# Performance work log

Measured on AMD Instinct MI355X. Metric: run time of the kernel, lower is better.

The kernel has to match this reference:

```python
import jax, jax.numpy as jnp
import numpy as np

N_HEADS = 8
NEG_INF = -1e30  # finite stand-in for -inf in masked_fill (exact 0 prob after softmax)


def apply_rotary_emb(x, cos, sin):
    # x: [B, H, T, hd]; cos/sin: [T, hd] -> broadcast over B, H
    d = x.shape[-1]
    x1, x2 = x[..., : d // 2], x[..., d // 2 :]
    x_rot = jnp.concatenate((-x2, x1), axis=-1)
    return x * cos[None, None] + x_rot * sin[None, None]


def setup_inputs() -> dict:
    key = jax.random.key(0)
    ks = jax.random.split(key, 5)
    B, T, C, hd = 4, 2048, 512, 64
    x = jax.random.normal(ks[0], (B, T, C), dtype=jnp.float32)
    cos = jax.random.uniform(ks[1], (T, hd), dtype=jnp.float32)
    sin = jax.random.uniform(ks[2], (T, hd), dtype=jnp.float32)
    # xavier_uniform-ish scale for linear weights
    W_qkv = jax.random.normal(ks[3], (3 * C, C), dtype=jnp.float32) * (1.0 / np.sqrt(C))
    W_out = jax.random.normal(ks[4], (C, C), dtype=jnp.float32) * (1.0 / np.sqrt(C))
    return {"x": x, "cos": cos, "sin": sin, "W_qkv": W_qkv, "W_out": W_out}


def reference(x, cos, sin, W_qkv, W_out):
    B, T, C = x.shape
    H = N_HEADS
    hd = C // H
    # qkv projection (torch Linear: y = x @ W^T), split into q, k, v as [B, H, T, hd]
    qkv = (x @ W_qkv.T).reshape(B, T, 3, H, hd)
    qkv = jnp.transpose(qkv, (2, 0, 3, 1, 4))
    q, k, v = qkv[0], qkv[1], qkv[2]
    # RoPE on q, k
    q = apply_rotary_emb(q, cos[:T], sin[:T])
    k = apply_rotary_emb(k, cos[:T], sin[:T])
    scale = jnp.sqrt(jnp.float32(hd))
    attn = jnp.einsum("bhqd,bhkd->bhqk", q, k) / scale  # [B, H, T, T]
    causal = jnp.tril(jnp.ones((T, T), dtype=bool))
    attn = jnp.where(causal[None, None], attn, NEG_INF)
    attn = jax.nn.softmax(attn, axis=-1)
    out = jnp.einsum("bhqk,bhkd->bhqd", attn, v)  # [B, H, T, hd]
    out = jnp.transpose(out, (0, 2, 1, 3)).reshape(B, T, C)
    return out @ W_out.T
```

## Files before the change

### kernel.cpp

```cpp
#include <hip/hip_runtime.h>
#include <hip/hip_bf16.h>
#include <math.h>

#define B_SZ 4
#define T_SZ 2048
#define C_SZ 512
#define H_SZ 8
#define HD 64
#define QSCALE 0.1803368801111137f

typedef __bf16 bf16;
typedef __bf16 bf16x8 __attribute__((ext_vector_type(8)));
typedef float f32x4 __attribute__((ext_vector_type(4)));

__device__ __forceinline__ f32x4 mfma16(bf16x8 a, bf16x8 b, f32x4 c) {
    return __builtin_amdgcn_mfma_f32_16x16x32_bf16(a, b, c, 0, 0, 0);
}

#define GLD_LDS16(g, l) __builtin_amdgcn_global_load_lds( \
    (__attribute__((address_space(1))) void*)(void*)(g),  \
    (__attribute__((address_space(3))) void*)(l), 16, 0, 0)

__global__ __launch_bounds__(256) void cvt_all(
    const float* __restrict__ x, const float* __restrict__ wqkv,
    const float* __restrict__ wout, bf16* __restrict__ xb,
    bf16* __restrict__ wqb, bf16* __restrict__ wob) {
  int i = blockIdx.x * 256 + threadIdx.x;
  const int n0 = (B_SZ*T_SZ*C_SZ)/4, n1 = (3*C_SZ*C_SZ)/4, n2 = (C_SZ*C_SZ)/4;
  const float4* s; bf16* d; int j;
  if (i < n0)                { s = (const float4*)x;    d = xb;  j = i; }
  else if (i < n0 + n1)      { s = (const float4*)wqkv; d = wqb; j = i - n0; }
  else if (i < n0 + n1 + n2) { s = (const float4*)wout; d = wob; j = i - n0 - n1; }
  else return;
  float4 v = s[j];
  union { bf16 h[4]; uint2 u; } p;
  p.h[0] = (bf16)v.x; p.h[1] = (bf16)v.y; p.h[2] = (bf16)v.z; p.h[3] = (bf16)v.w;
  *(uint2*)(d + (size_t)j * 4) = p.u;
}

__global__ __launch_bounds__(256) void gemm_qkv(
    const bf16* __restrict__ A, const bf16* __restrict__ Bw,
    const float* __restrict__ cp, const float* __restrict__ sp,
    bf16* __restrict__ oq, bf16* __restrict__ ok, bf16* __restrict__ ov) {
  __shared__ bf16 sA[128 * 32];
  __shared__ bf16 sB[128 * 32];
  const int tid = threadIdx.x;
  const int m0 = blockIdx.x * 128, n0 = blockIdx.y * 128;
  const int w = tid >> 6, lane = tid & 63, quad = lane >> 4, l16 = lane & 15;
  const int wm = (w >> 1) * 64, wn = (w & 1) * 64;
  const int srow = tid >> 2, scol = (tid & 3) * 8;
  const int K = C_SZ;
  f32x4 acc[4][4] = {};
  for (int k0 = 0; k0 < K; k0 += 32) {
    __syncthreads();
    const bf16* ga = A  + (size_t)(m0 + srow) * K + k0 + scol;
    const bf16* gb = Bw + (size_t)(n0 + srow) * K + k0 + scol;
    GLD_LDS16(ga,                 sA + tid * 8);
    GLD_LDS16(ga + (size_t)64*K,  sA + tid * 8 + 2048);
    GLD_LDS16(gb,                 sB + tid * 8);
    GLD_LDS16(gb + (size_t)64*K,  sB + tid * 8 + 2048);
    __syncthreads();
    bf16x8 af[4], bfr[4];
#pragma unroll
    for (int i = 0; i < 4; i++)
      af[i] = *(const bf16x8*)(sA + (wm + i*16 + l16) * 32 + quad * 8);
#pragma unroll
    for (int j = 0; j < 4; j++)
      bfr[j] = *(const bf16x8*)(sB + (wn + j*16 + l16) * 32 + quad * 8);
#pragma unroll
    for (int i = 0; i < 4; i++)
#pragma unroll
      for (int j = 0; j < 4; j++)
        acc[i][j] = mfma16(af[i], bfr[j], acc[i][j]);
  }
  const int three = n0 >> 9;
  if (three < 2) {
    bf16* dst0 = three == 0 ? oq : ok;
#pragma unroll
    for (int i = 0; i < 4; i++)
#pragma unroll
      for (int r = 0; r < 4; r++) {
        const int m = m0 + wm + i*16 + quad*4 + r;
        const int b = m >> 11, t = m & (T_SZ - 1);
#pragma unroll
        for (int j = 0; j < 2; j++) {
          const int dcol = j*16 + l16;
          const int h = ((n0 & 511) + wn + dcol) >> 6;
          const float c1 = cp[t*HD + dcol],     s1 = sp[t*HD + dcol];
          const float c2 = cp[t*HD + dcol + 32], s2 = sp[t*HD + dcol + 32];
          const float a = acc[i][j][r], bb = acc[i][j+2][r];
          float o1 = a * c1 - bb * s1;
          float o2 = bb * c2 + a * s2;
          if (three == 0) { o1 *= QSCALE; o2 *= QSCALE; }
          bf16* dst = dst0 + (((size_t)(b*H_SZ + h)) * T_SZ + t) * HD;
          dst[dcol]      = (bf16)o1;
          dst[dcol + 32] = (bf16)o2;
        }
      }
  } else {
#pragma unroll
    for (int i = 0; i < 4; i++)
#pragma unroll
      for (int j = 0; j < 4; j++) {
        const int n = n0 + wn + j*16 + l16;
        const int h = (n & 511) >> 6, dcol = n & 63;
#pragma unroll
        for (int r = 0; r < 4; r++) {
          const int m = m0 + wm + i*16 + quad*4 + r;
          const int b = m >> 11, t = m & (T_SZ - 1);
          ov[(((size_t)(b*H_SZ + h)) * HD + dcol) * T_SZ + t] = (bf16)acc[i][j][r];
        }
      }
  }
}

__global__ __launch_bounds__(256) void gemm_out(
    const bf16* __restrict__ A, const bf16* __restrict__ Bw,
    float* __restrict__ dst) {
  __shared__ bf16 sA[64 * 32];
  __shared__ bf16 sB[128 * 32];
  const int tid = threadIdx.x;
  const int m0 = blockIdx.x * 64, n0 = blockIdx.y * 128;
  const int w = tid >> 6, lane = tid & 63, quad = lane >> 4, l16 = lane & 15;
  const int wm = (w & 1) * 32, wn = (w >> 1) * 64;
  const int srow = tid >> 2, scol = (tid & 3) * 8;
  const int K = C_SZ;
  f32x4 acc[2][4] = {};
  for (int k0 = 0; k0 < K; k0 += 32) {
    __syncthreads();
    const bf16* ga = A  + (size_t)(m0 + srow) * K + k0 + scol;
    const bf16* gb = Bw + (size_t)(n0 + srow) * K + k0 + scol;
    GLD_LDS16(ga,                 sA + tid * 8);
    GLD_LDS16(gb,                 sB + tid * 8);
    GLD_LDS16(gb + (size_t)64*K,  sB + tid * 8 + 2048);
    __syncthreads();
    bf16x8 af[2], bfr[4];
#pragma unroll
    for (int i = 0; i < 2; i++)
      af[i] = *(const bf16x8*)(sA + (wm + i*16 + l16) * 32 + quad * 8);
#pragma unroll
    for (int j = 0; j < 4; j++)
      bfr[j] = *(const bf16x8*)(sB + (wn + j*16 + l16) * 32 + quad * 8);
#pragma unroll
    for (int i = 0; i < 2; i++)
#pragma unroll
      for (int j = 0; j < 4; j++)
        acc[i][j] = mfma16(af[i], bfr[j], acc[i][j]);
  }
#pragma unroll
  for (int i = 0; i < 2; i++)
#pragma unroll
    for (int j = 0; j < 4; j++)
#pragma unroll
      for (int r = 0; r < 4; r++) {
        const int m = m0 + wm + i*16 + quad*4 + r;
        const int n = n0 + wn + j*16 + l16;
        dst[(size_t)m * C_SZ + n] = acc[i][j][r];
      }
}

__device__ __forceinline__ int tile_of(int g) {
  int qi = (int)((sqrtf(4.f*(float)g + 1.f) - 1.f) * 0.5f);
  while ((qi + 1) * (qi + 2) <= g) ++qi;
  while (qi * (qi + 1) > g) --qi;
  return qi;
}

__global__ __launch_bounds__(256) void flash_attn(
    const bf16* __restrict__ qb, const bf16* __restrict__ kb,
    const bf16* __restrict__ vtb, bf16* __restrict__ Oa,
    float* __restrict__ lbuf) {
  __shared__ bf16 sK[2][64 * 64];
  __shared__ bf16 sVT[2][64 * 64];
  __shared__ bf16 sP[4][2560];
  const int tid = threadIdx.x, w = tid >> 6, lane = tid & 63;
  const int quad = lane >> 4, l16 = lane & 15;
  const int bh = blockIdx.x & 31;
  const int p  = blockIdx.x >> 5;
  const int gs = (34 * p) / 3, ge = (34 * (p + 1)) / 3;
  int qi = tile_of(gs);
  int tend = (qi + 1) * (qi + 2);
  int q0w = qi * 128 + w * 32;
  const bf16* Q  = qb  + (size_t)bh * T_SZ * HD;
  const bf16* Kp = kb  + (size_t)bh * T_SZ * HD;
  const bf16* Vt = vtb + (size_t)bh * HD * T_SZ;
  bf16x8 qf[2][2];
#pragma unroll
  for (int nt = 0; nt < 2; nt++)
#pragma unroll
    for (int ds = 0; ds < 2; ds++)
      qf[nt][ds] = *(const bf16x8*)(Q + (size_t)(q0w + nt*16 + l16) * HD + ds*32 + quad*8);
  float l_[2] = {0.f, 0.f};
  f32x4 ot[4][2] = {};
  bf16* sPw = &sP[w][0];
  const int srow = tid >> 3, scg = (tid & 7) ^ (srow & 7);

  auto partial_epilogue = [&]() {
    const int pf = (3 * qi * (qi + 1) + 2) / 34;
    const int rec = (bh * 16 + qi) * 4 + (p - pf);
#pragma unroll
    for (int nt = 0; nt < 2; nt++) {
      float s = l_[nt];
      s += __shfl_xor(s, 16);
      s += __shfl_xor(s, 32);
      if (quad == 0) lbuf[rec * 128 + w*32 + nt*16 + l16] = s;
    }
#pragma unroll
    for (int dt = 0; dt < 4; dt++)
#pragma unroll
      for (int nt = 0; nt < 2; nt++) {
        union { bf16 h4[4]; unsigned long long ull; } pk;
#pragma unroll
        for (int r = 0; r < 4; r++) pk.h4[r] = (bf16)ot[dt][nt][r];
        *(unsigned long long*)(sPw + (nt*16 + l16)*72 + dt*16 + quad*4) = pk.ull;
      }
    asm volatile("" ::: "memory");
    const int oq = lane >> 1, hf = lane & 1;
    bf16* dst = Oa + (size_t)rec * 8192 + (w*32 + oq) * 64 + hf * 32;
#pragma unroll
    for (int j = 0; j < 4; j++)
      *(uint4*)(dst + j*8) = *(const uint4*)(sPw + oq*72 + hf*32 + j*8);
    asm volatile("" ::: "memory");
  };

  {
    const int kt0 = (gs - qi * (qi + 1)) * 64;
    bf16* dK = sK[gs & 1];
    bf16* dV = sVT[gs & 1];
    GLD_LDS16(Kp + (size_t)(kt0 + srow) * HD + scg*8,        dK + tid*8);
    GLD_LDS16(Kp + (size_t)(kt0 + srow + 32) * HD + scg*8,   dK + tid*8 + 2048);
    GLD_LDS16(Vt + (size_t)srow * T_SZ + kt0 + scg*8,        dV + tid*8);
    GLD_LDS16(Vt + (size_t)(srow + 32) * T_SZ + kt0 + scg*8, dV + tid*8 + 2048);
  }

  for (int g = gs; g < ge; g++) {
    const int kt = (g - qi * (qi + 1)) * 64;
    __syncthreads();
    if (g + 1 < ge) {
      const int qn = (g + 1 >= tend) ? qi + 1 : qi;
      const int kn = (g + 1 - qn * (qn + 1)) * 64;
      bf16* dK = sK[(g + 1) & 1];
      bf16* dV = sVT[(g + 1) & 1];
      GLD_LDS16(Kp + (size_t)(kn + srow) * HD + scg*8,        dK + tid*8);
      GLD_LDS16(Kp + (size_t)(kn + srow + 32) * HD + scg*8,   dK + tid*8 + 2048);
      GLD_LDS16(Vt + (size_t)srow * T_SZ + kn + scg*8,        dV + tid*8);
      GLD_LDS16(Vt + (size_t)(srow + 32) * T_SZ + kn + scg*8, dV + tid*8 + 2048);
    }
    if (kt <= q0w + 31) {
      const bf16* cK = sK[g & 1];
      const bf16* cV = sVT[g & 1];
      f32x4 st[4][2] = {};
#pragma unroll
      for (int mt = 0; mt < 4; mt++) {
#pragma unroll
        for (int ds = 0; ds < 2; ds++) {
          const int row = mt*16 + l16, cl = ds*4 + quad;
          const bf16x8 kf = *(const bf16x8*)(cK + row*64 + (cl ^ (row & 7)) * 8);
#pragma unroll
          for (int nt = 0; nt < 2; nt++)
            st[mt][nt] = mfma16(kf, qf[nt][ds], st[mt][nt]);
        }
      }
      if (kt + 63 > q0w) {
#pragma unroll
        for (int nt = 0; nt < 2; nt++) {
          const int qg = q0w + nt*16 + l16;
          const int kb0 = kt + quad*4;
#pragma unroll
          for (int mt = 0; mt < 4; mt++)
#pragma unroll
            for (int r = 0; r < 4; r++)
              st[mt][nt][r] = (kb0 + mt*16 + r <= qg) ? st[mt][nt][r] : -1e30f;
        }
      }
#pragma unroll
      for (int nt = 0; nt < 2; nt++) {
        float sum = 0.f;
#pragma unroll
        for (int mt = 0; mt < 4; mt++) {
          union { bf16 h4[4]; unsigned long long ull; } pk;
#pragma unroll
          for (int r = 0; r < 4; r++) {
            const float pv = __builtin_amdgcn_exp2f(st[mt][nt][r]);
            sum += pv;
            pk.h4[r] = (bf16)pv;
          }
          *(unsigned long long*)(sPw + (mt>>1)*1280 + (nt*16 + l16)*40 + (mt&1)*16 + quad*4) = pk.ull;
        }
        l_[nt] += sum;
      }
      asm volatile("" ::: "memory");
      bf16x8 pfr[2][2];
#pragma unroll
      for (int nt = 0; nt < 2; nt++)
#pragma unroll
        for (int s = 0; s < 2; s++)
          pfr[nt][s] = *(const bf16x8*)(sPw + s*1280 + (nt*16 + l16)*40 + quad*8);
#pragma unroll
      for (int dt = 0; dt < 4; dt++) {
#pragma unroll
        for (int s = 0; s < 2; s++) {
          const int row = dt*16 + l16, cl = s*4 + quad;
          const bf16x8 vf = *(const bf16x8*)(cV + row*64 + (cl ^ (row & 7)) * 8);
#pragma unroll
          for (int nt = 0; nt < 2; nt++)
            ot[dt][nt] = mfma16(vf, pfr[nt][s], ot[dt][nt]);
        }
      }
    }
    if (g + 1 == tend || g + 1 == ge) {
      partial_epilogue();
      if (g + 1 == tend && g + 1 < ge) {
        qi++; tend = (qi + 1) * (qi + 2); q0w = qi * 128 + w * 32;
#pragma unroll
        for (int nt = 0; nt < 2; nt++)
#pragma unroll
          for (int ds = 0; ds < 2; ds++)
            qf[nt][ds] = *(const bf16x8*)(Q + (size_t)(q0w + nt*16 + l16) * HD + ds*32 + quad*8);
        l_[0] = 0.f; l_[1] = 0.f;
#pragma unroll
        for (int dt = 0; dt < 4; dt++)
#pragma unroll
          for (int nt = 0; nt < 2; nt++)
            ot[dt][nt] = f32x4{0.f, 0.f, 0.f, 0.f};
      }
    }
  }
}

__global__ __launch_bounds__(256) void combine_o(
    const bf16* __restrict__ Oa, const float* __restrict__ lbuf,
    bf16* __restrict__ ao) {
  const int inst = blockIdx.x;
  const int bh = inst & 31, qi = inst >> 5;
  const int b = bh >> 3, h = bh & 7;
  const int g0 = qi * (qi + 1), geL = (qi + 1) * (qi + 2) - 1;
  const int pf = (3 * g0 + 2) / 34, pl = (3 * geL + 2) / 34;
  const int n = pl - pf + 1;
  const int base = (bh * 16 + qi) * 4;
  const int t = threadIdx.x;
  const int q = t >> 1, d0 = (t & 1) * 32;
  float l = 0.f;
  for (int s = 0; s < n; s++) l += lbuf[(base + s) * 128 + q];
  const float inv = 1.f / l;
  float acc[32] = {};
  for (int s = 0; s < n; s++) {
    const bf16* ps = Oa + ((size_t)(base + s)) * 8192 + q * 64 + d0;
#pragma unroll
    for (int c = 0; c < 4; c++) {
      union { uint4 u; bf16 h8[8]; } a;
      a.u = *(const uint4*)(ps + c*8);
#pragma unroll
      for (int j = 0; j < 8; j++) acc[c*8 + j] += (float)a.h8[j];
    }
  }
  const int tg = qi * 128 + q;
  bf16* dst = ao + ((size_t)(b*T_SZ + tg)) * C_SZ + h*HD + d0;
#pragma unroll
  for (int c = 0; c < 4; c++) {
    union { uint4 u; bf16 h8[8]; } o;
#pragma unroll
    for (int j = 0; j < 8; j++) o.h8[j] = (bf16)(acc[c*8 + j] * inv);
    *(uint4*)(dst + c*8) = o.u;
  }
}

extern "C" void kernel_launch(void* const* d_in, const int* in_sizes, int n_in,
                              void* d_out, int out_size, void* d_ws, size_t ws_size,
                              hipStream_t stream) {
  const float* x    = (const float*)d_in[0];
  const float* cosp = (const float*)d_in[1];
  const float* sinp = (const float*)d_in[2];
  const float* wqkv = (const float*)d_in[3];
  const float* wout = (const float*)d_in[4];
  char* ws = (char*)d_ws;
  bf16* xb    = (bf16*)(ws);
  bf16* wqkvb = (bf16*)(ws +  8388608);
  bf16* woutb = (bf16*)(ws +  9961472);
  bf16* qbuf  = (bf16*)(ws + 10485760);
  bf16* kbuf  = (bf16*)(ws + 18874368);
  bf16* vtbuf = (bf16*)(ws + 27262976);
  bf16* ao    = (bf16*)(ws + 35651584);
  bf16* Oa    = (bf16*)(ws + 44040192);
  float* lbuf = (float*)(ws + 77594624);

  cvt_all<<<dim3(5120), dim3(256), 0, stream>>>(x, wqkv, wout, xb, wqkvb, woutb);
  gemm_qkv<<<dim3(64, 12), dim3(256), 0, stream>>>(
      xb, wqkvb, cosp, sinp, qbuf, kbuf, vtbuf);
  flash_attn<<<dim3(768), dim3(256), 0, stream>>>(qbuf, kbuf, vtbuf, Oa, lbuf);
  combine_o<<<dim3(512), dim3(256), 0, stream>>>(Oa, lbuf, ao);
  gemm_out<<<dim3(128, 4), dim3(256), 0, stream>>>(ao, woutb, (float*)d_out);
}
```

Measured before the change: 154.8 us.

## Retile flash attention to 256-query tiles with 32-key steps

The attention kernel now gives each block 256 query rows (64 per wave) and walks keys in 32-row steps, where before it used 128 query rows and 64-key steps. Work is split evenly at 12 steps per block, and the partial-output and combine layouts change to match. Larger query tiles reuse each K/V tile across more queries and cut the number of partial records that combine has to merge. The cost is more accumulator registers per wave, more frequent block-wide syncs per key, and a partial epilogue done in two halves; launch bounds request 3 blocks per CU.

```diff
diff --git a/kernel.cpp b/kernel.cpp
--- a/kernel.cpp
+++ b/kernel.cpp
@@ -160,124 +160,122 @@
 }
 
 __device__ __forceinline__ int tile_of(int g) {
-  int qi = (int)((sqrtf(4.f*(float)g + 1.f) - 1.f) * 0.5f);
-  while ((qi + 1) * (qi + 2) <= g) ++qi;
-  while (qi * (qi + 1) > g) --qi;
+  int qi = (int)((sqrtf((float)g + 1.f) - 1.f) * 0.5f);
+  while (4 * (qi + 1) * (qi + 2) <= g) ++qi;
+  while (4 * qi * (qi + 1) > g) --qi;
   return qi;
 }
 
-__global__ __launch_bounds__(256) void flash_attn(
+__global__ __launch_bounds__(256, 3) void flash_attn(
     const bf16* __restrict__ qb, const bf16* __restrict__ kb,
     const bf16* __restrict__ vtb, bf16* __restrict__ Oa,
     float* __restrict__ lbuf) {
-  __shared__ bf16 sK[2][64 * 64];
-  __shared__ bf16 sVT[2][64 * 64];
+  __shared__ bf16 sK[2][32 * 64];
+  __shared__ bf16 sVT[2][64 * 32];
   __shared__ bf16 sP[4][2560];
   const int tid = threadIdx.x, w = tid >> 6, lane = tid & 63;
   const int quad = lane >> 4, l16 = lane & 15;
   const int bh = blockIdx.x & 31;
   const int p  = blockIdx.x >> 5;
-  const int gs = (34 * p) / 3, ge = (34 * (p + 1)) / 3;
+  const int gs = 12 * p, ge = gs + 12;
   int qi = tile_of(gs);
-  int tend = (qi + 1) * (qi + 2);
-  int q0w = qi * 128 + w * 32;
+  int tend = 4 * (qi + 1) * (qi + 2);
+  int q0w = qi * 256 + w * 64;
   const bf16* Q  = qb  + (size_t)bh * T_SZ * HD;
   const bf16* Kp = kb  + (size_t)bh * T_SZ * HD;
   const bf16* Vt = vtb + (size_t)bh * HD * T_SZ;
-  bf16x8 qf[2][2];
-#pragma unroll
-  for (int nt = 0; nt < 2; nt++)
+  bf16x8 qf[4][2];
+#pragma unroll
+  for (int nt = 0; nt < 4; nt++)
 #pragma unroll
     for (int ds = 0; ds < 2; ds++)
       qf[nt][ds] = *(const bf16x8*)(Q + (size_t)(q0w + nt*16 + l16) * HD + ds*32 + quad*8);
-  float l_[2] = {0.f, 0.f};
-  f32x4 ot[4][2] = {};
+  float l_[4] = {0.f, 0.f, 0.f, 0.f};
+  f32x4 ot[4][4] = {};
   bf16* sPw = &sP[w][0];
   const int srow = tid >> 3, scg = (tid & 7) ^ (srow & 7);
+  const int vrow = tid >> 2, vcg = (tid & 3) ^ (vrow & 3);
 
   auto partial_epilogue = [&]() {
-    const int pf = (3 * qi * (qi + 1) + 2) / 34;
-    const int rec = (bh * 16 + qi) * 4 + (p - pf);
-#pragma unroll
-    for (int nt = 0; nt < 2; nt++) {
+    const int pf = (qi * (qi + 1)) / 3;
+    const int rec = (bh * 8 + qi) * 6 + (p - pf);
+#pragma unroll
+    for (int nt = 0; nt < 4; nt++) {
       float s = l_[nt];
       s += __shfl_xor(s, 16);
       s += __shfl_xor(s, 32);
-      if (quad == 0) lbuf[rec * 128 + w*32 + nt*16 + l16] = s;
-    }
-#pragma unroll
-    for (int dt = 0; dt < 4; dt++)
-#pragma unroll
-      for (int nt = 0; nt < 2; nt++) {
-        union { bf16 h4[4]; unsigned long long ull; } pk;
-#pragma unroll
-        for (int r = 0; r < 4; r++) pk.h4[r] = (bf16)ot[dt][nt][r];
-        *(unsigned long long*)(sPw + (nt*16 + l16)*72 + dt*16 + quad*4) = pk.ull;
-      }
-    asm volatile("" ::: "memory");
-    const int oq = lane >> 1, hf = lane & 1;
-    bf16* dst = Oa + (size_t)rec * 8192 + (w*32 + oq) * 64 + hf * 32;
-#pragma unroll
-    for (int j = 0; j < 4; j++)
-      *(uint4*)(dst + j*8) = *(const uint4*)(sPw + oq*72 + hf*32 + j*8);
+      if (quad == 0) lbuf[rec * 256 + w*64 + nt*16 + l16] = s;
+    }
+#pragma unroll
+    for (int h = 0; h < 2; h++) {
+      asm volatile("" ::: "memory");
+#pragma unroll
+      for (int dt = 0; dt < 4; dt++)
+#pragma unroll
+        for (int n2 = 0; n2 < 2; n2++) {
+          const int nt = h*2 + n2;
+          union { bf16 h4[4]; unsigned long long ull; } pk;
+#pragma unroll
+          for (int r = 0; r < 4; r++) pk.h4[r] = (bf16)ot[dt][nt][r];
+          *(unsigned long long*)(sPw + (n2*16 + l16)*72 + dt*16 + quad*4) = pk.ull;
+        }
+      asm volatile("" ::: "memory");
+      const int oq = lane >> 1, hf = lane & 1;
+      bf16* dst = Oa + (size_t)rec * 16384 + (w*64 + h*32 + oq) * 64 + hf * 32;
+#pragma unroll
+      for (int j = 0; j < 4; j++)
+        *(uint4*)(dst + j*8) = *(const uint4*)(sPw + oq*72 + hf*32 + j*8);
+    }
     asm volatile("" ::: "memory");
   };
 
   {
-    const int kt0 = (gs - qi * (qi + 1)) * 64;
-    bf16* dK = sK[gs & 1];
-    bf16* dV = sVT[gs & 1];
-    GLD_LDS16(Kp + (size_t)(kt0 + srow) * HD + scg*8,        dK + tid*8);
-    GLD_LDS16(Kp + (size_t)(kt0 + srow + 32) * HD + scg*8,   dK + tid*8 + 2048);
-    GLD_LDS16(Vt + (size_t)srow * T_SZ + kt0 + scg*8,        dV + tid*8);
-    GLD_LDS16(Vt + (size_t)(srow + 32) * T_SZ + kt0 + scg*8, dV + tid*8 + 2048);
+    const int kt0 = (gs - 4*qi*(qi+1)) * 32;
+    GLD_LDS16(Kp + (size_t)(kt0 + srow) * HD + scg*8, sK[gs & 1]  + tid*8);
+    GLD_LDS16(Vt + (size_t)vrow * T_SZ + kt0 + vcg*8, sVT[gs & 1] + tid*8);
   }
 
   for (int g = gs; g < ge; g++) {
-    const int kt = (g - qi * (qi + 1)) * 64;
+    const int kt = (g - 4*qi*(qi+1)) * 32;
     __syncthreads();
     if (g + 1 < ge) {
       const int qn = (g + 1 >= tend) ? qi + 1 : qi;
-      const int kn = (g + 1 - qn * (qn + 1)) * 64;
-      bf16* dK = sK[(g + 1) & 1];
-      bf16* dV = sVT[(g + 1) & 1];
-      GLD_LDS16(Kp + (size_t)(kn + srow) * HD + scg*8,        dK + tid*8);
-      GLD_LDS16(Kp + (size_t)(kn + srow + 32) * HD + scg*8,   dK + tid*8 + 2048);
-      GLD_LDS16(Vt + (size_t)srow * T_SZ + kn + scg*8,        dV + tid*8);
-      GLD_LDS16(Vt + (size_t)(srow + 32) * T_SZ + kn + scg*8, dV + tid*8 + 2048);
-    }
-    if (kt <= q0w + 31) {
+      const int kn = (g + 1 - 4*qn*(qn+1)) * 32;
+      GLD_LDS16(Kp + (size_t)(kn + srow) * HD + scg*8, sK[(g+1) & 1]  + tid*8);
+      GLD_LDS16(Vt + (size_t)vrow * T_SZ + kn + vcg*8, sVT[(g+1) & 1] + tid*8);
+    }
+    if (kt <= q0w + 63) {
       const bf16* cK = sK[g & 1];
       const bf16* cV = sVT[g & 1];
-      f32x4 st[4][2] = {};
-#pragma unroll
-      for (int mt = 0; mt < 4; mt++) {
+      f32x4 st[2][4] = {};
+#pragma unroll
+      for (int mt = 0; mt < 2; mt++) {
 #pragma unroll
         for (int ds = 0; ds < 2; ds++) {
           const int row = mt*16 + l16, cl = ds*4 + quad;
           const bf16x8 kf = *(const bf16x8*)(cK + row*64 + (cl ^ (row & 7)) * 8);
 #pragma unroll
-          for (int nt = 0; nt < 2; nt++)
+          for (int nt = 0; nt < 4; nt++)
             st[mt][nt] = mfma16(kf, qf[nt][ds], st[mt][nt]);
         }
       }
-      if (kt + 63 > q0w) {
-#pragma unroll
-        for (int nt = 0; nt < 2; nt++) {
+      if (kt + 31 > q0w) {
+#pragma unroll
+        for (int nt = 0; nt < 4; nt++) {
           const int qg = q0w + nt*16 + l16;
           const int kb0 = kt + quad*4;
 #pragma unroll
-          for (int mt = 0; mt < 4; mt++)
+          for (int mt = 0; mt < 2; mt++)
 #pragma unroll
             for (int r = 0; r < 4; r++)
               st[mt][nt][r] = (kb0 + mt*16 + r <= qg) ? st[mt][nt][r] : -1e30f;
         }
       }
 #pragma unroll
-      for (int nt = 0; nt < 2; nt++) {
+      for (int nt = 0; nt < 4; nt++) {
         float sum = 0.f;
 #pragma unroll
-        for (int mt = 0; mt < 4; mt++) {
+        for (int mt = 0; mt < 2; mt++) {
           union { bf16 h4[4]; unsigned long long ull; } pk;
 #pragma unroll
           for (int r = 0; r < 4; r++) {
@@ -285,43 +283,39 @@
             sum += pv;
             pk.h4[r] = (bf16)pv;
           }
-          *(unsigned long long*)(sPw + (mt>>1)*1280 + (nt*16 + l16)*40 + (mt&1)*16 + quad*4) = pk.ull;
+          *(unsigned long long*)(sPw + (nt*16 + l16)*40 + mt*16 + quad*4) = pk.ull;
         }
         l_[nt] += sum;
       }
       asm volatile("" ::: "memory");
-      bf16x8 pfr[2][2];
-#pragma unroll
-      for (int nt = 0; nt < 2; nt++)
-#pragma unroll
-        for (int s = 0; s < 2; s++)
-          pfr[nt][s] = *(const bf16x8*)(sPw + s*1280 + (nt*16 + l16)*40 + quad*8);
+      bf16x8 pfr[4];
+#pragma unroll
+      for (int nt = 0; nt < 4; nt++)
+        pfr[nt] = *(const bf16x8*)(sPw + (nt*16 + l16)*40 + quad*8);
 #pragma unroll
       for (int dt = 0; dt < 4; dt++) {
-#pragma unroll
-        for (int s = 0; s < 2; s++) {
-          const int row = dt*16 + l16, cl = s*4 + quad;
-          const bf16x8 vf = *(const bf16x8*)(cV + row*64 + (cl ^ (row & 7)) * 8);
-#pragma unroll
-          for (int nt = 0; nt < 2; nt++)
-            ot[dt][nt] = mfma16(vf, pfr[nt][s], ot[dt][nt]);
-        }
+        const int row = dt*16 + l16;
+        const bf16x8 vf = *(const bf16x8*)(cV + row*32 + (quad ^ (row & 3)) * 8);
+#pragma unroll
+        for (int nt = 0; nt < 4; nt++)
+          ot[dt][nt] = mfma16(vf, pfr[nt], ot[dt][nt]);
       }
     }
     if (g + 1 == tend || g + 1 == ge) {
       partial_epilogue();
       if (g + 1 == tend && g + 1 < ge) {
-        qi++; tend = (qi + 1) * (qi + 2); q0w = qi * 128 + w * 32;
-#pragma unroll
-        for (int nt = 0; nt < 2; nt++)
+        qi++; tend = 4 * (qi + 1) * (qi + 2); q0w = qi * 256 + w * 64;
+#pragma unroll
+        for (int nt = 0; nt < 4; nt++)
 #pragma unroll
           for (int ds = 0; ds < 2; ds++)
             qf[nt][ds] = *(const bf16x8*)(Q + (size_t)(q0w + nt*16 + l16) * HD + ds*32 + quad*8);
-        l_[0] = 0.f; l_[1] = 0.f;
+#pragma unroll
+        for (int nt = 0; nt < 4; nt++) l_[nt] = 0.f;
 #pragma unroll
         for (int dt = 0; dt < 4; dt++)
 #pragma unroll
-          for (int nt = 0; nt < 2; nt++)
+          for (int nt = 0; nt < 4; nt++)
             ot[dt][nt] = f32x4{0.f, 0.f, 0.f, 0.f};
       }
     }
@@ -334,30 +328,29 @@
   const int inst = blockIdx.x;
   const int bh = inst & 31, qi = inst >> 5;
   const int b = bh >> 3, h = bh & 7;
-  const int g0 = qi * (qi + 1), geL = (qi + 1) * (qi + 2) - 1;
-  const int pf = (3 * g0 + 2) / 34, pl = (3 * geL + 2) / 34;
+  const int g0 = 4 * qi * (qi + 1), gL = g0 + 8*qi + 7;
+  const int pf = g0 / 12, pl = gL / 12;
   const int n = pl - pf + 1;
-  const int base = (bh * 16 + qi) * 4;
-  const int t = threadIdx.x;
-  const int q = t >> 1, d0 = (t & 1) * 32;
+  const int base = (bh * 8 + qi) * 6;
+  const int q = threadIdx.x;
   float l = 0.f;
-  for (int s = 0; s < n; s++) l += lbuf[(base + s) * 128 + q];
+  for (int s = 0; s < n; s++) l += lbuf[(base + s) * 256 + q];
   const float inv = 1.f / l;
-  float acc[32] = {};
+  float acc[64] = {};
   for (int s = 0; s < n; s++) {
-    const bf16* ps = Oa + ((size_t)(base + s)) * 8192 + q * 64 + d0;
-#pragma unroll
-    for (int c = 0; c < 4; c++) {
+    const bf16* ps = Oa + ((size_t)(base + s)) * 16384 + q * 64;
+#pragma unroll
+    for (int c = 0; c < 8; c++) {
       union { uint4 u; bf16 h8[8]; } a;
       a.u = *(const uint4*)(ps + c*8);
 #pragma unroll
       for (int j = 0; j < 8; j++) acc[c*8 + j] += (float)a.h8[j];
     }
   }
-  const int tg = qi * 128 + q;
-  bf16* dst = ao + ((size_t)(b*T_SZ + tg)) * C_SZ + h*HD + d0;
-#pragma unroll
-  for (int c = 0; c < 4; c++) {
+  const int tg = qi * 256 + q;
+  bf16* dst = ao + ((size_t)(b*T_SZ + tg)) * C_SZ + h*HD;
+#pragma unroll
+  for (int c = 0; c < 8; c++) {
     union { uint4 u; bf16 h8[8]; } o;
 #pragma unroll
     for (int j = 0; j < 8; j++) o.h8[j] = (bf16)(acc[c*8 + j] * inv);
@@ -382,12 +375,12 @@
   bf16* vtbuf = (bf16*)(ws + 27262976);
   bf16* ao    = (bf16*)(ws + 35651584);
   bf16* Oa    = (bf16*)(ws + 44040192);
-  float* lbuf = (float*)(ws + 77594624);
+  float* lbuf = (float*)(ws + 94371840);
 
   cvt_all<<<dim3(5120), dim3(256), 0, stream>>>(x, wqkv, wout, xb, wqkvb, woutb);
   gemm_qkv<<<dim3(64, 12), dim3(256), 0, stream>>>(
       xb, wqkvb, cosp, sinp, qbuf, kbuf, vtbuf);
   flash_attn<<<dim3(768), dim3(256), 0, stream>>>(qbuf, kbuf, vtbuf, Oa, lbuf);
-  combine_o<<<dim3(512), dim3(256), 0, stream>>>(Oa, lbuf, ao);
+  combine_o<<<dim3(256), dim3(256), 0, stream>>>(Oa, lbuf, ao);
   gemm_out<<<dim3(128, 4), dim3(256), 0, stream>>>(ao, woutb, (float*)d_out);
 }
```

Result: slower. 166.2 us (+7.4%).
